# Optimization experiments

Measured on AMD Instinct MI355X. Metric: run time of the kernel, lower is better.

The kernel has to match this reference:

```python
import jax, jax.numpy as jnp
import numpy as np

N = 100000   # nodes
E = 640000   # directed edges
D = 128      # feature dim
C = 2        # classes


def setup_inputs() -> dict:
    key = jax.random.key(0)
    ks = jax.random.split(key, 7)
    s = 1.0 / np.sqrt(D)
    return {
        "x": jax.random.normal(ks[0], (N, D), jnp.float32),
        "edge_index": jax.random.randint(ks[1], (2, E), 0, N, jnp.int32),
        "W1": jax.random.normal(ks[2], (D, D), jnp.float32) * s,
        "b1": jnp.zeros((D,), jnp.float32),
        "W2": jax.random.normal(ks[3], (D, D), jnp.float32) * s,
        "b2": jnp.zeros((D,), jnp.float32),
        "Wfc": jax.random.normal(ks[4], (D, C), jnp.float32) * s,
        "bfc": jnp.zeros((C,), jnp.float32),
    }


def _gcn_conv(h, src, dst, W, b, n):
    """PyG GCNConv: y = D^{-1/2}(A+I)D^{-1/2} (h @ W) + b."""
    h = h @ W  # [N, D_out]
    loop = jnp.arange(n, dtype=src.dtype)
    s = jnp.concatenate([src, loop])
    d = jnp.concatenate([dst, loop])
    # degree of (A + I) counted at destination
    deg = jax.ops.segment_sum(jnp.ones_like(d, jnp.float32), d, num_segments=n)
    dinv = jax.lax.rsqrt(jnp.maximum(deg, 1.0))  # deg >= 1 via self loops
    norm = dinv[s] * dinv[d]                      # [E+N]
    msg = h[s] * norm[:, None]                    # gather + scale
    out = jax.ops.segment_sum(msg, d, num_segments=n)  # scatter-add
    return out + b


def reference(x, edge_index, W1, b1, W2, b2, Wfc, bfc):
    src, dst = edge_index[0], edge_index[1]
    n = x.shape[0]
    h = jax.nn.relu(_gcn_conv(x, src, dst, W1, b1, n))  # dropout = identity (eval)
    h = jax.nn.relu(_gcn_conv(h, src, dst, W2, b2, n))
    return h @ Wfc + bfc  # [N, 2] logits
```

## Files before the change

### kernel.cpp

```cpp
#include <hip/hip_runtime.h>
#include <hip/hip_bf16.h>

#define D 128
#define NBUCKET 64
#define BCAP 16384

typedef __bf16 bf16x8 __attribute__((ext_vector_type(8)));
typedef float f32x4 __attribute__((ext_vector_type(4)));


__global__ void prep_kernel(const float* __restrict__ W1, const float* __restrict__ W2,
                            __bf16* __restrict__ pw, int* __restrict__ bucket_cursor,
                            int* __restrict__ deghist) {
    int b = blockIdx.x;
    if (b < 128) {
        int t = b * 256 + threadIdx.x;
        int which = t >> 14, idx = t & 16383;
        const float* W = which ? W2 : W1;
        float w = W[idx];
        int k = idx >> 7, nn = idx & 127;
        int ks = which ? (((k & 15) << 3) | (k >> 4)) : k;
        int ntile = nn >> 4, nl = nn & 15;
        int kchunk = ks >> 5, quad = (ks >> 3) & 3, j = ks & 7;
        int o = (((ntile * 4 + kchunk) * 64 + quad * 16 + nl) << 3) + j;
        pw[(size_t)which * 16384 + o] = (__bf16)w;
    } else {
        int t = threadIdx.x;
        if (t < NBUCKET) bucket_cursor[t] = 0;
        else if (t < 128) deghist[t - 64] = 0;
    }
}

__global__ void mega1_kernel(const float* __restrict__ X, const __bf16* __restrict__ PW,
                             __bf16* __restrict__ Zs, int nrows, int gb,
                             const int* __restrict__ src, const int* __restrict__ dst,
                             int* __restrict__ bucket_cursor, int2* __restrict__ bucket_edges,
                             int e, int bucketW) {
    __shared__ __align__(16) char smem[32768];
    int t = threadIdx.x;
    int b = blockIdx.x;
    if (b >= gb) {
        int* hist = (int*)smem;
        int* gbase = hist + 64;
        if (t < NBUCKET) hist[t] = 0;
        __syncthreads();
        int i0 = ((b - gb) * 256 + t) * 4;
        int sv[4], dv[4], bk[4], ls[4];
        int nv = 0;
        if (i0 + 4 <= e) {
            int4 s4 = *(const int4*)(src + i0);
            int4 d4 = *(const int4*)(dst + i0);
            sv[0] = s4.x; sv[1] = s4.y; sv[2] = s4.z; sv[3] = s4.w;
            dv[0] = d4.x; dv[1] = d4.y; dv[2] = d4.z; dv[3] = d4.w;
            nv = 4;
        } else {
            for (int i = i0; i < e; i++) { sv[nv] = src[i]; dv[nv] = dst[i]; nv++; }
        }
        for (int u = 0; u < nv; u++) {
            bk[u] = dv[u] / bucketW;
            ls[u] = atomicAdd(&hist[bk[u]], 1);
        }
        __syncthreads();
        if (t < NBUCKET) gbase[t] = atomicAdd(&bucket_cursor[t], hist[t]);
        __syncthreads();
        for (int u = 0; u < nv; u++) {
            int pos = bk[u] * BCAP + gbase[bk[u]] + ls[u];
            bucket_edges[pos] = make_int2(sv[u], dv[u]);
        }
        return;
    }
    bf16x8* sB = (bf16x8*)smem;
    const bf16x8* PW8 = (const bf16x8*)PW;
#pragma unroll
    for (int i = 0; i < 8; i++) sB[t + 256 * i] = PW8[t + 256 * i];

    int wave = t >> 6, lane = t & 63;
    int qm = lane & 15, quad = lane >> 4;
    int r0 = b * 64 + wave * 16;
    int row = r0 + qm;
    bool valid = row < nrows;
    const float* xr = X + (size_t)row * D + quad * 8;

    bf16x8 ahi[4], alo[4];
#pragma unroll
    for (int c = 0; c < 4; c++) {
        float4 zf = {0.f, 0.f, 0.f, 0.f};
        float4 xa = valid ? ((const float4*)(xr + c * 32))[0] : zf;
        float4 xb = valid ? ((const float4*)(xr + c * 32))[1] : zf;
        float xs[8] = {xa.x, xa.y, xa.z, xa.w, xb.x, xb.y, xb.z, xb.w};
        bf16x8 h, l;
#pragma unroll
        for (int j = 0; j < 8; j++) {
            float v = xs[j];
            __bf16 hh = (__bf16)v;
            h[j] = hh;
            l[j] = (__bf16)(v - (float)hh);
        }
        ahi[c] = h; alo[c] = l;
    }

    f32x4 acc[8];
#pragma unroll
    for (int nt = 0; nt < 8; nt++) acc[nt] = (f32x4){0.f, 0.f, 0.f, 0.f};

    __syncthreads();

#pragma unroll
    for (int c = 0; c < 4; c++) {
#pragma unroll
        for (int nt = 0; nt < 8; nt++) {
            bf16x8 bb = sB[(nt * 4 + c) * 64 + lane];
            acc[nt] = __builtin_amdgcn_mfma_f32_16x16x32_bf16(ahi[c], bb, acc[nt], 0, 0, 0);
            acc[nt] = __builtin_amdgcn_mfma_f32_16x16x32_bf16(alo[c], bb, acc[nt], 0, 0, 0);
        }
    }

#pragma unroll
    for (int reg = 0; reg < 4; reg++) {
        int orow = r0 + quad * 4 + reg;
        if (orow < nrows) {
            bf16x8 o;
#pragma unroll
            for (int nt = 0; nt < 8; nt++) o[nt] = (__bf16)acc[nt][reg];
            *(bf16x8*)(Zs + (size_t)orow * D + qm * 8) = o;
        }
    }
}

__global__ void count2_kernel(const int2* __restrict__ bucket_edges,
                              const int* __restrict__ bucket_cursor,
                              int* __restrict__ counts, float* __restrict__ dinv,
                              int* __restrict__ partial, int* __restrict__ deghist,
                              int n, int bucketW, int subW) {
    __shared__ int bins[400];
    __shared__ int sm[256];
    __shared__ int hb[64];
    int b = blockIdx.x, t = threadIdx.x;
    int bk = b >> 2, j = b & 3;
    int ns = bk * bucketW + j * subW;
    int be = min((bk + 1) * bucketW, n);
    int ne = min(ns + subW, be);
    int w = ne - ns;
    if (w <= 0) { if (t == 0) partial[b] = 0; return; }
    for (int i = t; i < w; i += 256) bins[i] = 0;
    if (t < 64) hb[t] = 0;
    __syncthreads();
    int m = bucket_cursor[bk];
    const int2* eb = bucket_edges + (size_t)bk * BCAP;
    for (int i = t; i < m; i += 256) {
        int d = eb[i].y;
        if (d >= ns && d < ne) atomicAdd(&bins[d - ns], 1);
    }
    __syncthreads();
    int s = 0;
    for (int i = t; i < w; i += 256) {
        int c = bins[i];
        counts[ns + i] = c;
        dinv[ns + i] = rsqrtf((float)(c + 1));
        atomicAdd(&hb[min(c, 63)], 1);
        s += c;
    }
    sm[t] = s; __syncthreads();
    for (int off = 128; off > 0; off >>= 1) { if (t < off) sm[t] += sm[t + off]; __syncthreads(); }
    if (t == 0) partial[b] = sm[0];
    if (t < 64 && hb[t]) atomicAdd(&deghist[t], hb[t]);
}

__global__ void scan_top(int* partial, int* deghist, int* degcur, int nb) {
    __shared__ int sm[256];
    int t = threadIdx.x;
    int v = (t < nb) ? partial[t] : 0;
    sm[t] = v; __syncthreads();
    for (int off = 1; off < 256; off <<= 1) {
        int u = (t >= off) ? sm[t - off] : 0;
        __syncthreads();
        sm[t] += u;
        __syncthreads();
    }
    if (t < nb) partial[t] = sm[t] - v;
    __syncthreads();
    int d = (t < 64) ? deghist[t] : 0;
    sm[t] = d; __syncthreads();
    for (int off = 1; off < 64; off <<= 1) {
        int u = (t >= off && t < 64) ? sm[t - off] : 0;
        __syncthreads();
        if (t < 64) sm[t] += u;
        __syncthreads();
    }
    if (t < 64) degcur[t] = sm[t] - d;
}

__global__ void scanfill_kernel(const int2* __restrict__ bucket_edges,
                                const int* __restrict__ bucket_cursor,
                                const int* __restrict__ counts,
                                const int* __restrict__ partial,
                                int* __restrict__ row_ptr, int* __restrict__ csr,
                                int* __restrict__ degcur, int* __restrict__ order,
                                int n, int bucketW, int subW) {
    __shared__ int cur[400];
    __shared__ int sm[256];
    __shared__ int hb2[64];
    __shared__ int gb2[64];
    int b = blockIdx.x, t = threadIdx.x;
    int bk = b >> 2, j = b & 3;
    int ns = bk * bucketW + j * subW;
    int be = min((bk + 1) * bucketW, n);
    int ne = min(ns + subW, be);
    int w = ne - ns;
    if (w <= 0) return;
    if (t < 64) hb2[t] = 0;
    int i0 = t * 2;
    int c0 = (i0 < w) ? counts[ns + i0] : 0;
    int c1 = (i0 + 1 < w) ? counts[ns + i0 + 1] : 0;
    sm[t] = c0 + c1; __syncthreads();
    int own = c0 + c1;
    for (int off = 1; off < 256; off <<= 1) {
        int u = (t >= off) ? sm[t - off] : 0;
        __syncthreads();
        sm[t] += u;
        __syncthreads();
    }
    int base = partial[b] + sm[t] - own;
    if (i0 < w)     { row_ptr[ns + i0] = base;          cur[i0] = base; }
    if (i0 + 1 < w) { row_ptr[ns + i0 + 1] = base + c0; cur[i0 + 1] = base + c0; }
    int bin0 = min(c0, 63), bin1 = min(c1, 63);
    int r0 = (i0 < w) ? atomicAdd(&hb2[bin0], 1) : 0;
    int r1 = (i0 + 1 < w) ? atomicAdd(&hb2[bin1], 1) : 0;
    __syncthreads();
    if (t < 64 && hb2[t]) gb2[t] = atomicAdd(&degcur[t], hb2[t]);
    __syncthreads();
    if (i0 < w)     order[gb2[bin0] + r0] = ns + i0;
    if (i0 + 1 < w) order[gb2[bin1] + r1] = ns + i0 + 1;
    __syncthreads();
    int m = bucket_cursor[bk];
    const int2* eb = bucket_edges + (size_t)bk * BCAP;
    for (int i = t; i < m; i += 256) {
        int2 ed = eb[i];
        if (ed.y >= ns && ed.y < ne) {
            int pos = atomicAdd(&cur[ed.y - ns], 1);
            csr[pos] = ed.x;
        }
    }
}

__global__ void agg1_gemm2_kernel(const __bf16* __restrict__ Zs, const int* __restrict__ row_ptr,
                                  const int* __restrict__ counts, const int* __restrict__ csr,
                                  const float* __restrict__ dinv, const float* __restrict__ bias,
                                  const __bf16* __restrict__ PW, const int* __restrict__ order,
                                  __bf16* __restrict__ Z2, int n) {
    __shared__ __align__(16) __bf16 sH[32 * 128];
    __shared__ bf16x8 sBp[512];
    int t = threadIdx.x;
    const bf16x8* PW8 = (const bf16x8*)PW;

    int gbase = blockIdx.x * 32;
    int grp = t >> 4, c = t & 15;

    float bs[8];
#pragma unroll
    for (int j = 0; j < 8; j++) bs[j] = bias[j * 16 + c];

    const bf16x8* Z8 = (const bf16x8*)Zs;
    for (int r = 0; r < 4; r++) {
        int lr = r * 8 + grp;
        int idx = gbase + lr;
        bf16x8 o = {};
        if (idx < n) {
            int v = order[(n - 1) - idx];
            float dv = dinv[v];
            bf16x8 zc = Z8[(size_t)v * 16 + c];
            float sw = dv * dv;
            float acc[8];
#pragma unroll
            for (int j = 0; j < 8; j++) acc[j] = (float)zc[j] * sw;
            int start = row_ptr[v], cnt = counts[v];
            int i = 0;
            if (cnt >= 4) {
                int s0 = csr[start], s1 = csr[start + 1];
                int s2 = csr[start + 2], s3 = csr[start + 3];
                for (; i + 8 <= cnt; i += 4) {
                    int t0 = csr[start + i + 4], t1 = csr[start + i + 5];
                    int t2 = csr[start + i + 6], t3 = csr[start + i + 7];
                    bf16x8 m0 = Z8[(size_t)s0 * 16 + c];
                    bf16x8 m1 = Z8[(size_t)s1 * 16 + c];
                    bf16x8 m2 = Z8[(size_t)s2 * 16 + c];
                    bf16x8 m3 = Z8[(size_t)s3 * 16 + c];
                    float w0 = dinv[s0] * dv, w1 = dinv[s1] * dv;
                    float w2 = dinv[s2] * dv, w3 = dinv[s3] * dv;
#pragma unroll
                    for (int j = 0; j < 8; j++) acc[j] = fmaf(w0, (float)m0[j], acc[j]);
#pragma unroll
                    for (int j = 0; j < 8; j++) acc[j] = fmaf(w1, (float)m1[j], acc[j]);
#pragma unroll
                    for (int j = 0; j < 8; j++) acc[j] = fmaf(w2, (float)m2[j], acc[j]);
#pragma unroll
                    for (int j = 0; j < 8; j++) acc[j] = fmaf(w3, (float)m3[j], acc[j]);
                    s0 = t0; s1 = t1; s2 = t2; s3 = t3;
                }
                {
                    bf16x8 m0 = Z8[(size_t)s0 * 16 + c];
                    bf16x8 m1 = Z8[(size_t)s1 * 16 + c];
                    bf16x8 m2 = Z8[(size_t)s2 * 16 + c];
                    bf16x8 m3 = Z8[(size_t)s3 * 16 + c];
                    float w0 = dinv[s0] * dv, w1 = dinv[s1] * dv;
                    float w2 = dinv[s2] * dv, w3 = dinv[s3] * dv;
#pragma unroll
                    for (int j = 0; j < 8; j++) acc[j] = fmaf(w0, (float)m0[j], acc[j]);
#pragma unroll
                    for (int j = 0; j < 8; j++) acc[j] = fmaf(w1, (float)m1[j], acc[j]);
#pragma unroll
                    for (int j = 0; j < 8; j++) acc[j] = fmaf(w2, (float)m2[j], acc[j]);
#pragma unroll
                    for (int j = 0; j < 8; j++) acc[j] = fmaf(w3, (float)m3[j], acc[j]);
                    i += 4;
                }
            }
            for (; i < cnt; i++) {
                int s0 = csr[start + i];
                float w0 = dinv[s0] * dv;
                bf16x8 m0 = Z8[(size_t)s0 * 16 + c];
#pragma unroll
                for (int j = 0; j < 8; j++) acc[j] = fmaf(w0, (float)m0[j], acc[j]);
            }
#pragma unroll
            for (int j = 0; j < 8; j++) o[j] = (__bf16)fmaxf(acc[j] + bs[j], 0.f);
        }
        *(bf16x8*)(sH + lr * 128 + ((c ^ (lr & 7)) << 3)) = o;
    }

    int wave = t >> 6, lane = t & 63;
    int qm = lane & 15, quad = lane >> 4;
    int lrow = wave * 16 + qm;

    f32x4 acc[8];
#pragma unroll
    for (int nt = 0; nt < 8; nt++) acc[nt] = (f32x4){0.f, 0.f, 0.f, 0.f};

#pragma unroll
    for (int cc = 0; cc < 4; cc++) {
        __syncthreads();
#pragma unroll
        for (int i = 0; i < 4; i++) {
            int idx = i * 128 + t;
            sBp[idx] = PW8[((idx >> 6) * 4 + cc) * 64 + (idx & 63)];
        }
        int slot = quad + cc * 4;
        bf16x8 a = *(const bf16x8*)(sH + lrow * 128 + ((slot ^ (lrow & 7)) << 3));
        __syncthreads();
#pragma unroll
        for (int nt = 0; nt < 8; nt++) {
            bf16x8 bb = sBp[nt * 64 + lane];
            acc[nt] = __builtin_amdgcn_mfma_f32_16x16x32_bf16(a, bb, acc[nt], 0, 0, 0);
        }
    }

#pragma unroll
    for (int reg = 0; reg < 4; reg++) {
        int lrr = wave * 16 + quad * 4 + reg;
        int gidx = gbase + lrr;
        if (gidx < n) {
            int v = order[(n - 1) - gidx];
            float sc = dinv[v];
            bf16x8 o;
#pragma unroll
            for (int nt = 0; nt < 8; nt++) o[nt] = (__bf16)(acc[nt][reg] * sc);
            *(bf16x8*)(Z2 + (size_t)v * D + qm * 8) = o;
        }
    }
}

__global__ void agg2_fc_kernel(const __bf16* __restrict__ Zs, const int* __restrict__ row_ptr,
                               const int* __restrict__ counts, const int* __restrict__ csr,
                               const float* __restrict__ dinv, const float* __restrict__ bias,
                               const float* __restrict__ Wfc, const float* __restrict__ bfc,
                               const int* __restrict__ order, float* __restrict__ out, int n) {
    int t = blockIdx.x * 256 + threadIdx.x;
    int idx = t >> 4, c = t & 15;
    if (idx >= n) return;
    int v = order[(n - 1) - idx];
    float dv = dinv[v];
    const bf16x8* Z8 = (const bf16x8*)Zs;
    bf16x8 zc = Z8[(size_t)v * 16 + c];
    float acc[8];
#pragma unroll
    for (int j = 0; j < 8; j++) acc[j] = (float)zc[j];
    int start = row_ptr[v], cnt = counts[v];
    int i = 0;
    if (cnt >= 4) {
        int s0 = csr[start], s1 = csr[start + 1];
        int s2 = csr[start + 2], s3 = csr[start + 3];
        for (; i + 8 <= cnt; i += 4) {
            int t0 = csr[start + i + 4], t1 = csr[start + i + 5];
            int t2 = csr[start + i + 6], t3 = csr[start + i + 7];
            bf16x8 m0 = Z8[(size_t)s0 * 16 + c];
            bf16x8 m1 = Z8[(size_t)s1 * 16 + c];
            bf16x8 m2 = Z8[(size_t)s2 * 16 + c];
            bf16x8 m3 = Z8[(size_t)s3 * 16 + c];
#pragma unroll
            for (int j = 0; j < 8; j++) acc[j] += (float)m0[j];
#pragma unroll
            for (int j = 0; j < 8; j++) acc[j] += (float)m1[j];
#pragma unroll
            for (int j = 0; j < 8; j++) acc[j] += (float)m2[j];
#pragma unroll
            for (int j = 0; j < 8; j++) acc[j] += (float)m3[j];
            s0 = t0; s1 = t1; s2 = t2; s3 = t3;
        }
        {
            bf16x8 m0 = Z8[(size_t)s0 * 16 + c];
            bf16x8 m1 = Z8[(size_t)s1 * 16 + c];
            bf16x8 m2 = Z8[(size_t)s2 * 16 + c];
            bf16x8 m3 = Z8[(size_t)s3 * 16 + c];
#pragma unroll
            for (int j = 0; j < 8; j++) acc[j] += (float)m0[j];
#pragma unroll
            for (int j = 0; j < 8; j++) acc[j] += (float)m1[j];
#pragma unroll
            for (int j = 0; j < 8; j++) acc[j] += (float)m2[j];
#pragma unroll
            for (int j = 0; j < 8; j++) acc[j] += (float)m3[j];
            i += 4;
        }
    }
    for (; i < cnt; i++) {
        int s0 = csr[start + i];
        bf16x8 m0 = Z8[(size_t)s0 * 16 + c];
#pragma unroll
        for (int j = 0; j < 8; j++) acc[j] += (float)m0[j];
    }
    float a0 = 0.f, a1 = 0.f;
#pragma unroll
    for (int j = 0; j < 8; j++) {
        int p = j * 16 + c;
        float hj = fmaxf(fmaf(dv, acc[j], bias[p]), 0.f);
        a0 = fmaf(hj, Wfc[p * 2], a0);
        a1 = fmaf(hj, Wfc[p * 2 + 1], a1);
    }
#pragma unroll
    for (int off = 8; off > 0; off >>= 1) {
        a0 += __shfl_down(a0, off, 16);
        a1 += __shfl_down(a1, off, 16);
    }
    if (c == 0) {
        out[(size_t)v * 2 + 0] = a0 + bfc[0];
        out[(size_t)v * 2 + 1] = a1 + bfc[1];
    }
}


extern "C" void kernel_launch(void* const* d_in, const int* in_sizes, int n_in,
                              void* d_out, int out_size, void* d_ws, size_t ws_size,
                              hipStream_t stream) {
    const float* x   = (const float*)d_in[0];
    const int*   ei  = (const int*)d_in[1];
    const float* W1  = (const float*)d_in[2];
    const float* b1  = (const float*)d_in[3];
    const float* W2  = (const float*)d_in[4];
    const float* b2  = (const float*)d_in[5];
    const float* Wfc = (const float*)d_in[6];
    const float* bfc = (const float*)d_in[7];
    float* out = (float*)d_out;

    int n = in_sizes[0] / D;
    int e = in_sizes[1] / 2;
    const int* src = ei;
    const int* dst = ei + e;

    int bucketW = (n + NBUCKET - 1) / NBUCKET;
    int subW = (bucketW + 3) / 4;

    char* ws = (char*)d_ws;
    size_t nb = (size_t)n * 4;
    int*    counts  = (int*)(ws);
    float*  dinv    = (float*)(ws + nb);
    int*    rowptr  = (int*)(ws + 2 * nb);
    int*    partial = (int*)(ws + 3 * nb);
    int*    bcur    = (int*)(ws + 3 * nb + 1024);
    int*    deghist = (int*)(ws + 3 * nb + 1280);
    int*    degcur  = (int*)(ws + 3 * nb + 1536);
    int*    order   = (int*)(ws + 3 * nb + 2048);
    int2*   bedges  = (int2*)(ws + 4 * nb + 2048);
    size_t  off1    = 4 * nb + 2048 + (size_t)NBUCKET * BCAP * 8;
    int*    csr     = (int*)(ws + off1);
    __bf16* pw      = (__bf16*)(ws + off1 + (size_t)e * 4);
    __bf16* z1      = (__bf16*)(ws + off1 + (size_t)e * 4 + 65536);
    __bf16* z2      = z1 + (size_t)n * D;

    int eab = ((e + 3) / 4 + 255) / 256;
    int gb  = (n + 63) / 64;
    int gb2 = (n + 31) / 32;
    int ab  = ((n * 16) + 255) / 256;

    prep_kernel<<<129, 256, 0, stream>>>(W1, W2, pw, bcur, deghist);
    mega1_kernel<<<gb + eab, 256, 0, stream>>>(x, pw, z1, n, gb, src, dst,
                                               bcur, bedges, e, bucketW);
    count2_kernel<<<256, 256, 0, stream>>>(bedges, bcur, counts, dinv, partial, deghist,
                                           n, bucketW, subW);
    scan_top<<<1, 256, 0, stream>>>(partial, deghist, degcur, 256);
    scanfill_kernel<<<256, 256, 0, stream>>>(bedges, bcur, counts, partial, rowptr, csr,
                                             degcur, order, n, bucketW, subW);
    agg1_gemm2_kernel<<<gb2, 128, 0, stream>>>(z1, rowptr, counts, csr, dinv, b1,
                                               pw + 16384, order, z2, n);
    agg2_fc_kernel<<<ab, 256, 0, stream>>>(z2, rowptr, counts, csr, dinv, b2, Wfc, bfc,
                                           order, out, n);
}
```

Before: 233.1 us.

## Move GEMM1 after degree count and pre-scale rows by dinv to drop per-edge weights

The first GEMM moves out of the bucketize launch and into a combined launch with the CSR scan/fill, after degrees are known. Each output row of X@W1 is now pre-multiplied by its dinv, so layer-1 aggregation becomes a plain sum of gathered rows followed by one multiply by the destination's dinv. This removes the per-edge dinv gathers and multiplies in agg1. The trade-off is that the GEMM no longer overlaps with bucketization, and rounding to bf16 after scaling changes numerics slightly.

```diff
diff --git a/kernel.cpp b/kernel.cpp
--- a/kernel.cpp
+++ b/kernel.cpp
@@ -31,99 +31,36 @@
     }
 }
 
-__global__ void mega1_kernel(const float* __restrict__ X, const __bf16* __restrict__ PW,
-                             __bf16* __restrict__ Zs, int nrows, int gb,
-                             const int* __restrict__ src, const int* __restrict__ dst,
-                             int* __restrict__ bucket_cursor, int2* __restrict__ bucket_edges,
-                             int e, int bucketW) {
-    __shared__ __align__(16) char smem[32768];
+__global__ void bucketize_kernel(const int* __restrict__ src, const int* __restrict__ dst,
+                                 int* __restrict__ bucket_cursor, int2* __restrict__ bucket_edges,
+                                 int e, int bucketW) {
+    __shared__ int hist[NBUCKET];
+    __shared__ int gbase[NBUCKET];
     int t = threadIdx.x;
-    int b = blockIdx.x;
-    if (b >= gb) {
-        int* hist = (int*)smem;
-        int* gbase = hist + 64;
-        if (t < NBUCKET) hist[t] = 0;
-        __syncthreads();
-        int i0 = ((b - gb) * 256 + t) * 4;
-        int sv[4], dv[4], bk[4], ls[4];
-        int nv = 0;
-        if (i0 + 4 <= e) {
-            int4 s4 = *(const int4*)(src + i0);
-            int4 d4 = *(const int4*)(dst + i0);
-            sv[0] = s4.x; sv[1] = s4.y; sv[2] = s4.z; sv[3] = s4.w;
-            dv[0] = d4.x; dv[1] = d4.y; dv[2] = d4.z; dv[3] = d4.w;
-            nv = 4;
-        } else {
-            for (int i = i0; i < e; i++) { sv[nv] = src[i]; dv[nv] = dst[i]; nv++; }
-        }
-        for (int u = 0; u < nv; u++) {
-            bk[u] = dv[u] / bucketW;
-            ls[u] = atomicAdd(&hist[bk[u]], 1);
-        }
-        __syncthreads();
-        if (t < NBUCKET) gbase[t] = atomicAdd(&bucket_cursor[t], hist[t]);
-        __syncthreads();
-        for (int u = 0; u < nv; u++) {
-            int pos = bk[u] * BCAP + gbase[bk[u]] + ls[u];
-            bucket_edges[pos] = make_int2(sv[u], dv[u]);
-        }
-        return;
-    }
-    bf16x8* sB = (bf16x8*)smem;
-    const bf16x8* PW8 = (const bf16x8*)PW;
-#pragma unroll
-    for (int i = 0; i < 8; i++) sB[t + 256 * i] = PW8[t + 256 * i];
-
-    int wave = t >> 6, lane = t & 63;
-    int qm = lane & 15, quad = lane >> 4;
-    int r0 = b * 64 + wave * 16;
-    int row = r0 + qm;
-    bool valid = row < nrows;
-    const float* xr = X + (size_t)row * D + quad * 8;
-
-    bf16x8 ahi[4], alo[4];
-#pragma unroll
-    for (int c = 0; c < 4; c++) {
-        float4 zf = {0.f, 0.f, 0.f, 0.f};
-        float4 xa = valid ? ((const float4*)(xr + c * 32))[0] : zf;
-        float4 xb = valid ? ((const float4*)(xr + c * 32))[1] : zf;
-        float xs[8] = {xa.x, xa.y, xa.z, xa.w, xb.x, xb.y, xb.z, xb.w};
-        bf16x8 h, l;
-#pragma unroll
-        for (int j = 0; j < 8; j++) {
-            float v = xs[j];
-            __bf16 hh = (__bf16)v;
-            h[j] = hh;
-            l[j] = (__bf16)(v - (float)hh);
-        }
-        ahi[c] = h; alo[c] = l;
-    }
-
-    f32x4 acc[8];
-#pragma unroll
-    for (int nt = 0; nt < 8; nt++) acc[nt] = (f32x4){0.f, 0.f, 0.f, 0.f};
-
-    __syncthreads();
-
-#pragma unroll
-    for (int c = 0; c < 4; c++) {
-#pragma unroll
-        for (int nt = 0; nt < 8; nt++) {
-            bf16x8 bb = sB[(nt * 4 + c) * 64 + lane];
-            acc[nt] = __builtin_amdgcn_mfma_f32_16x16x32_bf16(ahi[c], bb, acc[nt], 0, 0, 0);
-            acc[nt] = __builtin_amdgcn_mfma_f32_16x16x32_bf16(alo[c], bb, acc[nt], 0, 0, 0);
-        }
-    }
-
-#pragma unroll
-    for (int reg = 0; reg < 4; reg++) {
-        int orow = r0 + quad * 4 + reg;
-        if (orow < nrows) {
-            bf16x8 o;
-#pragma unroll
-            for (int nt = 0; nt < 8; nt++) o[nt] = (__bf16)acc[nt][reg];
-            *(bf16x8*)(Zs + (size_t)orow * D + qm * 8) = o;
-        }
+    if (t < NBUCKET) hist[t] = 0;
+    __syncthreads();
+    int i0 = (blockIdx.x * 256 + t) * 4;
+    int sv[4], dv[4], bk[4], ls[4];
+    int nv = 0;
+    if (i0 + 4 <= e) {
+        int4 s4 = *(const int4*)(src + i0);
+        int4 d4 = *(const int4*)(dst + i0);
+        sv[0] = s4.x; sv[1] = s4.y; sv[2] = s4.z; sv[3] = s4.w;
+        dv[0] = d4.x; dv[1] = d4.y; dv[2] = d4.z; dv[3] = d4.w;
+        nv = 4;
+    } else {
+        for (int i = i0; i < e; i++) { sv[nv] = src[i]; dv[nv] = dst[i]; nv++; }
+    }
+    for (int u = 0; u < nv; u++) {
+        bk[u] = dv[u] / bucketW;
+        ls[u] = atomicAdd(&hist[bk[u]], 1);
+    }
+    __syncthreads();
+    if (t < NBUCKET) gbase[t] = atomicAdd(&bucket_cursor[t], hist[t]);
+    __syncthreads();
+    for (int u = 0; u < nv; u++) {
+        int pos = bk[u] * BCAP + gbase[bk[u]] + ls[u];
+        bucket_edges[pos] = make_int2(sv[u], dv[u]);
     }
 }
 
@@ -190,55 +127,120 @@
     if (t < 64) degcur[t] = sm[t] - d;
 }
 
-__global__ void scanfill_kernel(const int2* __restrict__ bucket_edges,
-                                const int* __restrict__ bucket_cursor,
-                                const int* __restrict__ counts,
-                                const int* __restrict__ partial,
-                                int* __restrict__ row_ptr, int* __restrict__ csr,
-                                int* __restrict__ degcur, int* __restrict__ order,
-                                int n, int bucketW, int subW) {
-    __shared__ int cur[400];
-    __shared__ int sm[256];
-    __shared__ int hb2[64];
-    __shared__ int gb2[64];
-    int b = blockIdx.x, t = threadIdx.x;
-    int bk = b >> 2, j = b & 3;
-    int ns = bk * bucketW + j * subW;
-    int be = min((bk + 1) * bucketW, n);
-    int ne = min(ns + subW, be);
-    int w = ne - ns;
-    if (w <= 0) return;
-    if (t < 64) hb2[t] = 0;
-    int i0 = t * 2;
-    int c0 = (i0 < w) ? counts[ns + i0] : 0;
-    int c1 = (i0 + 1 < w) ? counts[ns + i0 + 1] : 0;
-    sm[t] = c0 + c1; __syncthreads();
-    int own = c0 + c1;
-    for (int off = 1; off < 256; off <<= 1) {
-        int u = (t >= off) ? sm[t - off] : 0;
-        __syncthreads();
-        sm[t] += u;
-        __syncthreads();
-    }
-    int base = partial[b] + sm[t] - own;
-    if (i0 < w)     { row_ptr[ns + i0] = base;          cur[i0] = base; }
-    if (i0 + 1 < w) { row_ptr[ns + i0 + 1] = base + c0; cur[i0 + 1] = base + c0; }
-    int bin0 = min(c0, 63), bin1 = min(c1, 63);
-    int r0 = (i0 < w) ? atomicAdd(&hb2[bin0], 1) : 0;
-    int r1 = (i0 + 1 < w) ? atomicAdd(&hb2[bin1], 1) : 0;
-    __syncthreads();
-    if (t < 64 && hb2[t]) gb2[t] = atomicAdd(&degcur[t], hb2[t]);
-    __syncthreads();
-    if (i0 < w)     order[gb2[bin0] + r0] = ns + i0;
-    if (i0 + 1 < w) order[gb2[bin1] + r1] = ns + i0 + 1;
-    __syncthreads();
-    int m = bucket_cursor[bk];
-    const int2* eb = bucket_edges + (size_t)bk * BCAP;
-    for (int i = t; i < m; i += 256) {
-        int2 ed = eb[i];
-        if (ed.y >= ns && ed.y < ne) {
-            int pos = atomicAdd(&cur[ed.y - ns], 1);
-            csr[pos] = ed.x;
+__global__ void mega2_kernel(const int2* __restrict__ bucket_edges,
+                             const int* __restrict__ bucket_cursor,
+                             const int* __restrict__ counts,
+                             const int* __restrict__ partial,
+                             int* __restrict__ row_ptr, int* __restrict__ csr,
+                             int* __restrict__ degcur, int* __restrict__ order,
+                             const float* __restrict__ X, const __bf16* __restrict__ PW,
+                             const float* __restrict__ dinv, __bf16* __restrict__ Zs,
+                             int n, int bucketW, int subW, int sfb) {
+    __shared__ __align__(16) char smem[32768];
+    int t = threadIdx.x;
+    int b = blockIdx.x;
+    if (b < sfb) {
+        int* cur = (int*)smem;
+        int* sm  = cur + 400;
+        int* hb2 = sm + 256;
+        int* gb2 = hb2 + 64;
+        int bk = b >> 2, j = b & 3;
+        int ns = bk * bucketW + j * subW;
+        int be = min((bk + 1) * bucketW, n);
+        int ne = min(ns + subW, be);
+        int w = ne - ns;
+        if (w <= 0) return;
+        if (t < 64) hb2[t] = 0;
+        int i0 = t * 2;
+        int c0 = (i0 < w) ? counts[ns + i0] : 0;
+        int c1 = (i0 + 1 < w) ? counts[ns + i0 + 1] : 0;
+        sm[t] = c0 + c1; __syncthreads();
+        int own = c0 + c1;
+        for (int off = 1; off < 256; off <<= 1) {
+            int u = (t >= off) ? sm[t - off] : 0;
+            __syncthreads();
+            sm[t] += u;
+            __syncthreads();
+        }
+        int base = partial[b] + sm[t] - own;
+        if (i0 < w)     { row_ptr[ns + i0] = base;          cur[i0] = base; }
+        if (i0 + 1 < w) { row_ptr[ns + i0 + 1] = base + c0; cur[i0 + 1] = base + c0; }
+        int bin0 = min(c0, 63), bin1 = min(c1, 63);
+        int r0 = (i0 < w) ? atomicAdd(&hb2[bin0], 1) : 0;
+        int r1 = (i0 + 1 < w) ? atomicAdd(&hb2[bin1], 1) : 0;
+        __syncthreads();
+        if (t < 64 && hb2[t]) gb2[t] = atomicAdd(&degcur[t], hb2[t]);
+        __syncthreads();
+        if (i0 < w)     order[gb2[bin0] + r0] = ns + i0;
+        if (i0 + 1 < w) order[gb2[bin1] + r1] = ns + i0 + 1;
+        __syncthreads();
+        int m = bucket_cursor[bk];
+        const int2* eb = bucket_edges + (size_t)bk * BCAP;
+        for (int i = t; i < m; i += 256) {
+            int2 ed = eb[i];
+            if (ed.y >= ns && ed.y < ne) {
+                int pos = atomicAdd(&cur[ed.y - ns], 1);
+                csr[pos] = ed.x;
+            }
+        }
+        return;
+    }
+    int gbk = b - sfb;
+    bf16x8* sB = (bf16x8*)smem;
+    const bf16x8* PW8 = (const bf16x8*)PW;
+#pragma unroll
+    for (int i = 0; i < 8; i++) sB[t + 256 * i] = PW8[t + 256 * i];
+
+    int wave = t >> 6, lane = t & 63;
+    int qm = lane & 15, quad = lane >> 4;
+    int r0 = gbk * 64 + wave * 16;
+    int row = r0 + qm;
+    bool valid = row < n;
+    const float* xr = X + (size_t)row * D + quad * 8;
+
+    bf16x8 ahi[4], alo[4];
+#pragma unroll
+    for (int c = 0; c < 4; c++) {
+        float4 zf = {0.f, 0.f, 0.f, 0.f};
+        float4 xa = valid ? ((const float4*)(xr + c * 32))[0] : zf;
+        float4 xb = valid ? ((const float4*)(xr + c * 32))[1] : zf;
+        float xs[8] = {xa.x, xa.y, xa.z, xa.w, xb.x, xb.y, xb.z, xb.w};
+        bf16x8 h, l;
+#pragma unroll
+        for (int j = 0; j < 8; j++) {
+            float v = xs[j];
+            __bf16 hh = (__bf16)v;
+            h[j] = hh;
+            l[j] = (__bf16)(v - (float)hh);
+        }
+        ahi[c] = h; alo[c] = l;
+    }
+
+    f32x4 acc[8];
+#pragma unroll
+    for (int nt = 0; nt < 8; nt++) acc[nt] = (f32x4){0.f, 0.f, 0.f, 0.f};
+
+    __syncthreads();
+
+#pragma unroll
+    for (int c = 0; c < 4; c++) {
+#pragma unroll
+        for (int nt = 0; nt < 8; nt++) {
+            bf16x8 bb = sB[(nt * 4 + c) * 64 + lane];
+            acc[nt] = __builtin_amdgcn_mfma_f32_16x16x32_bf16(ahi[c], bb, acc[nt], 0, 0, 0);
+            acc[nt] = __builtin_amdgcn_mfma_f32_16x16x32_bf16(alo[c], bb, acc[nt], 0, 0, 0);
+        }
+    }
+
+#pragma unroll
+    for (int reg = 0; reg < 4; reg++) {
+        int orow = r0 + quad * 4 + reg;
+        if (orow < n) {
+            float sc = dinv[orow];
+            bf16x8 o;
+#pragma unroll
+            for (int nt = 0; nt < 8; nt++) o[nt] = (__bf16)(acc[nt][reg] * sc);
+            *(bf16x8*)(Zs + (size_t)orow * D + qm * 8) = o;
         }
     }
 }
@@ -269,10 +271,9 @@
             int v = order[(n - 1) - idx];
             float dv = dinv[v];
             bf16x8 zc = Z8[(size_t)v * 16 + c];
-            float sw = dv * dv;
             float acc[8];
 #pragma unroll
-            for (int j = 0; j < 8; j++) acc[j] = (float)zc[j] * sw;
+            for (int j = 0; j < 8; j++) acc[j] = (float)zc[j];
             int start = row_ptr[v], cnt = counts[v];
             int i = 0;
             if (cnt >= 4) {
@@ -285,16 +286,14 @@
                     bf16x8 m1 = Z8[(size_t)s1 * 16 + c];
                     bf16x8 m2 = Z8[(size_t)s2 * 16 + c];
                     bf16x8 m3 = Z8[(size_t)s3 * 16 + c];
-                    float w0 = dinv[s0] * dv, w1 = dinv[s1] * dv;
-                    float w2 = dinv[s2] * dv, w3 = dinv[s3] * dv;
-#pragma unroll
-                    for (int j = 0; j < 8; j++) acc[j] = fmaf(w0, (float)m0[j], acc[j]);
-#pragma unroll
-                    for (int j = 0; j < 8; j++) acc[j] = fmaf(w1, (float)m1[j], acc[j]);
-#pragma unroll
-                    for (int j = 0; j < 8; j++) acc[j] = fmaf(w2, (float)m2[j], acc[j]);
-#pragma unroll
-                    for (int j = 0; j < 8; j++) acc[j] = fmaf(w3, (float)m3[j], acc[j]);
+#pragma unroll
+                    for (int j = 0; j < 8; j++) acc[j] += (float)m0[j];
+#pragma unroll
+                    for (int j = 0; j < 8; j++) acc[j] += (float)m1[j];
+#pragma unroll
+                    for (int j = 0; j < 8; j++) acc[j] += (float)m2[j];
+#pragma unroll
+                    for (int j = 0; j < 8; j++) acc[j] += (float)m3[j];
                     s0 = t0; s1 = t1; s2 = t2; s3 = t3;
                 }
                 {
@@ -302,28 +301,25 @@
                     bf16x8 m1 = Z8[(size_t)s1 * 16 + c];
                     bf16x8 m2 = Z8[(size_t)s2 * 16 + c];
                     bf16x8 m3 = Z8[(size_t)s3 * 16 + c];
-                    float w0 = dinv[s0] * dv, w1 = dinv[s1] * dv;
-                    float w2 = dinv[s2] * dv, w3 = dinv[s3] * dv;
-#pragma unroll
-                    for (int j = 0; j < 8; j++) acc[j] = fmaf(w0, (float)m0[j], acc[j]);
-#pragma unroll
-                    for (int j = 0; j < 8; j++) acc[j] = fmaf(w1, (float)m1[j], acc[j]);
-#pragma unroll
-                    for (int j = 0; j < 8; j++) acc[j] = fmaf(w2, (float)m2[j], acc[j]);
-#pragma unroll
-                    for (int j = 0; j < 8; j++) acc[j] = fmaf(w3, (float)m3[j], acc[j]);
+#pragma unroll
+                    for (int j = 0; j < 8; j++) acc[j] += (float)m0[j];
+#pragma unroll
+                    for (int j = 0; j < 8; j++) acc[j] += (float)m1[j];
+#pragma unroll
+                    for (int j = 0; j < 8; j++) acc[j] += (float)m2[j];
+#pragma unroll
+                    for (int j = 0; j < 8; j++) acc[j] += (float)m3[j];
                     i += 4;
                 }
             }
             for (; i < cnt; i++) {
                 int s0 = csr[start + i];
-                float w0 = dinv[s0] * dv;
                 bf16x8 m0 = Z8[(size_t)s0 * 16 + c];
 #pragma unroll
-                for (int j = 0; j < 8; j++) acc[j] = fmaf(w0, (float)m0[j], acc[j]);
+                for (int j = 0; j < 8; j++) acc[j] += (float)m0[j];
             }
 #pragma unroll
-            for (int j = 0; j < 8; j++) o[j] = (__bf16)fmaxf(acc[j] + bs[j], 0.f);
+            for (int j = 0; j < 8; j++) o[j] = (__bf16)fmaxf(fmaf(dv, acc[j], bs[j]), 0.f);
         }
         *(bf16x8*)(sH + lr * 128 + ((c ^ (lr & 7)) << 3)) = o;
     }
@@ -490,15 +486,16 @@
     int gb  = (n + 63) / 64;
     int gb2 = (n + 31) / 32;
     int ab  = ((n * 16) + 255) / 256;
+    int sfb = 256;
 
     prep_kernel<<<129, 256, 0, stream>>>(W1, W2, pw, bcur, deghist);
-    mega1_kernel<<<gb + eab, 256, 0, stream>>>(x, pw, z1, n, gb, src, dst,
-                                               bcur, bedges, e, bucketW);
+    bucketize_kernel<<<eab, 256, 0, stream>>>(src, dst, bcur, bedges, e, bucketW);
     count2_kernel<<<256, 256, 0, stream>>>(bedges, bcur, counts, dinv, partial, deghist,
                                            n, bucketW, subW);
     scan_top<<<1, 256, 0, stream>>>(partial, deghist, degcur, 256);
-    scanfill_kernel<<<256, 256, 0, stream>>>(bedges, bcur, counts, partial, rowptr, csr,
-                                             degcur, order, n, bucketW, subW);
+    mega2_kernel<<<sfb + gb, 256, 0, stream>>>(bedges, bcur, counts, partial, rowptr, csr,
+                                               degcur, order, x, pw, dinv, z1,
+                                               n, bucketW, subW, sfb);
     agg1_gemm2_kernel<<<gb2, 128, 0, stream>>>(z1, rowptr, counts, csr, dinv, b1,
                                                pw + 16384, order, z2, n);
     agg2_fc_kernel<<<ab, 256, 0, stream>>>(z2, rowptr, counts, csr, dinv, b2, Wfc, bfc,
```

Result: no change. 235.9 us (+1.2%).
